# Kernel optimization log

Hardware: AMD Instinct MI355X
Metric: run time of the kernel (lower is better)

The kernel has to match this reference:

```python
import jax, jax.numpy as jnp
import numpy as np

N_HEADS = 4
DIM_HEAD = 32


def setup_inputs() -> dict:
    key = jax.random.key(0)
    k1, k2, k3, k4 = jax.random.split(key, 4)
    x = jax.random.normal(k1, (8, 64, 80, 1024), dtype=jnp.float32)
    # conv_qkv: 1x1 conv, no bias -> weight [3*heads*dim_head, dim_in_out]
    w_qkv = jax.random.normal(k2, (3 * N_HEADS * DIM_HEAD, 64), dtype=jnp.float32) * 0.05
    # conv_out: 1x1 conv with bias -> weight [dim_in_out, heads*dim_head], bias [dim_in_out]
    w_out = jax.random.normal(k3, (64, N_HEADS * DIM_HEAD), dtype=jnp.float32) * 0.05
    b_out = jax.random.normal(k4, (64,), dtype=jnp.float32) * 0.05
    return {"x": x, "w_qkv": w_qkv, "w_out": w_out, "b_out": b_out}


def reference(x, w_qkv, w_out, b_out):
    b, c, h, w = x.shape
    n = h * w
    # 1x1 conv == channel matmul
    qkv = jnp.einsum('bchw,oc->bohw', x, w_qkv)            # [b, 3*heads*dh, h, w]
    qkv = qkv.reshape(b, 3, N_HEADS, DIM_HEAD, n)          # qkv outermost, then heads, then c
    q, k, v = qkv[:, 0], qkv[:, 1], qkv[:, 2]              # each [b, heads, dh, n]
    k = jax.nn.softmax(k, axis=-1)                          # softmax over spatial positions
    context = jnp.einsum('bhdn,bhen->bhde', k, v)          # [b, heads, dh, dh]
    out = jnp.einsum('bhde,bhdn->bhen', context, q)        # [b, heads, dh, n]
    out = out.reshape(b, N_HEADS * DIM_HEAD, h, w)
    return jnp.einsum('bchw,oc->bohw', out, w_out) + b_out[None, :, None, None]
```

## Files before the change

kernel.cpp:

```cpp
#include <hip/hip_runtime.h>
#include <stdint.h>


#define N_POS 81920
#define NT    128
#define TILES 640

typedef short bf16x8 __attribute__((ext_vector_type(8)));
typedef float f32x4  __attribute__((ext_vector_type(4)));

__device__ __forceinline__ uint32_t packbf(float lo, float hi){
  uint32_t a = __float_as_uint(lo), b = __float_as_uint(hi);
  a = (a + 0x8000u) >> 16;
  b = (b + 0x8000u) & 0xffff0000u;
  return a | b;
}
__device__ __forceinline__ short bf16of(float v){
  return (short)((__float_as_uint(v) + 0x8000u) >> 16);
}

__global__ __launch_bounds__(512, 4) void kernA(
    const float* __restrict__ x, const float* __restrict__ w,
    float* __restrict__ pA, float* __restrict__ pZ, int nch, int tpc)
{
  __shared__ __align__(16) uint16_t xs_cp[64 * 136];
  __shared__ __align__(16) uint16_t xs_pc[128 * 72];
  __shared__ __align__(16) uint16_t es[128 * 136];

  const int t  = threadIdx.x;
  const int w8 = t >> 6;
  const int l  = t & 63;
  const int lm = l & 15;
  const int lg = l >> 4;

  const int b  = blockIdx.x / nch;
  const int ch = blockIdx.x % nch;
  const float* xb = x + (size_t)b * 64 * N_POS;

  const int rr  = t >> 3;
  const int pg  = t & 7;
  const int spp = t & 127;
  const int scg = t >> 7;

  const int pth = w8 & 3;
  const int ht0 = (w8 >> 2) * 4;

  bf16x8 wkf[4][2];
  #pragma unroll
  for (int i = 0; i < 4; ++i)
    #pragma unroll
    for (int kk = 0; kk < 2; ++kk){
      const float* wp = w + (size_t)(128 + 16*(ht0+i) + lm) * 64 + 32*kk + 8*lg;
      float4 w0 = *(const float4*)wp;
      float4 w1 = *(const float4*)(wp + 4);
      bf16x8 f;
      f[0]=bf16of(w0.x); f[1]=bf16of(w0.y); f[2]=bf16of(w0.z); f[3]=bf16of(w0.w);
      f[4]=bf16of(w1.x); f[5]=bf16of(w1.y); f[6]=bf16of(w1.z); f[7]=bf16of(w1.w);
      wkf[i][kk] = f;
    }

  bf16x8 ones;
  #pragma unroll
  for (int j = 0; j < 8; ++j) ones[j] = (short)0x3F80;

  f32x4 acc[4], zac;
  zac = (f32x4){0.f,0.f,0.f,0.f};
  #pragma unroll
  for (int n = 0; n < 4; ++n) acc[n] = (f32x4){0.f,0.f,0.f,0.f};

  float4 fa0, fa1, fa2, fa3;
  float v[16];
  {
    const int n0 = (ch * tpc) * NT;
    const float* ga = xb + (size_t)rr * N_POS + n0 + 16*pg;
    fa0 = *(const float4*)ga;       fa1 = *(const float4*)(ga + 4);
    fa2 = *(const float4*)(ga + 8); fa3 = *(const float4*)(ga + 12);
    const float* gb = xb + (size_t)(16*scg) * N_POS + n0 + spp;
    #pragma unroll
    for (int i = 0; i < 16; ++i) v[i] = gb[(size_t)i * N_POS];
  }

  for (int tile = 0; tile < tpc; ++tile){
    __syncthreads();
    {
      uint4 u0, u1;
      u0.x = packbf(fa0.x,fa0.y); u0.y = packbf(fa0.z,fa0.w);
      u0.z = packbf(fa1.x,fa1.y); u0.w = packbf(fa1.z,fa1.w);
      u1.x = packbf(fa2.x,fa2.y); u1.y = packbf(fa2.z,fa2.w);
      u1.z = packbf(fa3.x,fa3.y); u1.w = packbf(fa3.z,fa3.w);
      *(uint4*)&xs_cp[rr*136 + 16*pg]     = u0;
      *(uint4*)&xs_cp[rr*136 + 16*pg + 8] = u1;
      uint4 p0, p1;
      p0.x = packbf(v[0],v[1]);   p0.y = packbf(v[2],v[3]);
      p0.z = packbf(v[4],v[5]);   p0.w = packbf(v[6],v[7]);
      p1.x = packbf(v[8],v[9]);   p1.y = packbf(v[10],v[11]);
      p1.z = packbf(v[12],v[13]); p1.w = packbf(v[14],v[15]);
      *(uint4*)&xs_pc[spp*72 + 16*scg]     = p0;
      *(uint4*)&xs_pc[spp*72 + 16*scg + 8] = p1;
    }
    __syncthreads();
    if (tile + 1 < tpc){
      const int n1 = (ch * tpc + tile + 1) * NT;
      const float* ga = xb + (size_t)rr * N_POS + n1 + 16*pg;
      fa0 = *(const float4*)ga;       fa1 = *(const float4*)(ga + 4);
      fa2 = *(const float4*)(ga + 8); fa3 = *(const float4*)(ga + 12);
      const float* gb = xb + (size_t)(16*scg) * N_POS + n1 + spp;
      #pragma unroll
      for (int i = 0; i < 16; ++i) v[i] = gb[(size_t)i * N_POS];
    }
    #pragma unroll
    for (int ip = 0; ip < 2; ++ip){
      const int pt = pth + 4*ip;
      bf16x8 af0 = *(const bf16x8*)&xs_pc[(16*pt + lm)*72 + 8*lg];
      bf16x8 af1 = *(const bf16x8*)&xs_pc[(16*pt + lm)*72 + 32 + 8*lg];
      #pragma unroll
      for (int i = 0; i < 4; ++i){
        f32x4 s = (f32x4){0.f,0.f,0.f,0.f};
        s = __builtin_amdgcn_mfma_f32_16x16x32_bf16(af0, wkf[i][0], s, 0,0,0);
        s = __builtin_amdgcn_mfma_f32_16x16x32_bf16(af1, wkf[i][1], s, 0,0,0);
        float e0 = __expf(s[0]), e1 = __expf(s[1]);
        float e2 = __expf(s[2]), e3 = __expf(s[3]);
        uint2 pk; pk.x = packbf(e0,e1); pk.y = packbf(e2,e3);
        *(uint2*)&es[(16*(ht0+i) + lm)*136 + 16*pt + 4*lg] = pk;
      }
    }
    __syncthreads();
    __builtin_amdgcn_s_setprio(1);
    #pragma unroll
    for (int kk = 0; kk < 4; ++kk){
      bf16x8 ea = *(const bf16x8*)&es[(16*w8 + lm)*136 + 32*kk + 8*lg];
      bf16x8 xbf[4];
      #pragma unroll
      for (int n = 0; n < 4; ++n)
        xbf[n] = *(const bf16x8*)&xs_cp[(16*n + lm)*136 + 32*kk + 8*lg];
      #pragma unroll
      for (int n = 0; n < 4; ++n)
        acc[n] = __builtin_amdgcn_mfma_f32_16x16x32_bf16(ea, xbf[n], acc[n], 0,0,0);
      zac = __builtin_amdgcn_mfma_f32_16x16x32_bf16(ea, ones, zac, 0,0,0);
    }
    __builtin_amdgcn_s_setprio(0);
  }

  float* pa = pA + (size_t)blockIdx.x * 8192;
  const int hd0 = 16*w8 + 4*lg;
  #pragma unroll
  for (int n = 0; n < 4; ++n)
    #pragma unroll
    for (int r = 0; r < 4; ++r)
      pa[(size_t)(hd0 + r)*64 + 16*n + lm] = acc[n][r];
  if (lm == 0){
    #pragma unroll
    for (int r = 0; r < 4; ++r)
      pZ[(size_t)blockIdx.x * 128 + hd0 + r] = zac[r];
  }
}

__global__ __launch_bounds__(256) void kernR1(
    const float* __restrict__ pA, const float* __restrict__ pZ,
    float* __restrict__ Ar, float* __restrict__ Zr, int nch)
{
  const int b = blockIdx.x >> 3, s = blockIdx.x & 7;
  const int off = s * 1024 + threadIdx.x * 4;
  float4 a = make_float4(0.f, 0.f, 0.f, 0.f);
  for (int ch = 0; ch < nch; ++ch){
    float4 v = *(const float4*)&pA[(size_t)(b * nch + ch) * 8192 + off];
    a.x += v.x; a.y += v.y; a.z += v.z; a.w += v.w;
  }
  *(float4*)&Ar[(size_t)b * 8192 + off] = a;
  if (s == 0 && threadIdx.x < 128){
    float z = 0.f;
    for (int ch = 0; ch < nch; ++ch) z += pZ[(size_t)(b * nch + ch) * 128 + threadIdx.x];
    Zr[b * 128 + threadIdx.x] = z;
  }
}

__global__ __launch_bounds__(256) void kernCM(
    const float* __restrict__ Ar, const float* __restrict__ Zr,
    const float* __restrict__ w_qkv, const float* __restrict__ w_out,
    float* __restrict__ M)
{
  __shared__ float A[128 * 65];
  __shared__ float Z[128];
  __shared__ float cs[128 * 33];
  __shared__ float T[64 * 129];
  const int b = blockIdx.x, t = threadIdx.x;

  #pragma unroll
  for (int k = 0; k < 32; ++k){
    int i = t + 256 * k;
    A[(i >> 6) * 65 + (i & 63)] = Ar[(size_t)b * 8192 + i];
  }
  if (t < 128) Z[t] = Zr[b * 128 + t];
  __syncthreads();

  {
    const int hd = t & 127, h = hd >> 5, e0 = (t >> 7) * 16;
    const float rz = 1.0f / Z[hd];
    for (int je = 0; je < 16; ++je){
      int e = e0 + je;
      const float* wv = w_qkv + (size_t)(256 + 32 * h + e) * 64;
      float a = 0.f;
      #pragma unroll
      for (int c = 0; c < 64; ++c) a = fmaf(A[hd * 65 + c], wv[c], a);
      cs[hd * 33 + e] = a * rz;
    }
  }
  __syncthreads();

  const int o = t & 63, g = t >> 6;
  for (int jh = 0; jh < 32; ++jh){
    int hd = 32 * g + jh;
    const float* wo = w_out + (size_t)o * 128 + 32 * g;
    float a = 0.f;
    #pragma unroll
    for (int e = 0; e < 32; ++e) a = fmaf(wo[e], cs[hd * 33 + e], a);
    T[o * 129 + hd] = a;
  }
  __syncthreads();

  const int c0 = 16 * g;
  float m[16];
  #pragma unroll
  for (int j = 0; j < 16; ++j) m[j] = 0.f;
  for (int hd = 0; hd < 128; ++hd){
    float tv = T[o * 129 + hd];
    const float* wq = w_qkv + (size_t)hd * 64 + c0;
    #pragma unroll
    for (int j = 0; j < 16; ++j) m[j] = fmaf(tv, wq[j], m[j]);
  }
  #pragma unroll
  for (int j = 0; j < 16; ++j) M[(size_t)b * 4096 + o * 64 + c0 + j] = m[j];
}

__global__ __launch_bounds__(256, 4) void kernO(
    const float* __restrict__ x, const float* __restrict__ M,
    const float* __restrict__ b_out, float* __restrict__ out)
{
  const int t  = threadIdx.x;
  const int wv = t >> 6;
  const int l  = t & 63;
  const int lm = l & 15;
  const int lg = l >> 4;

  const int b  = blockIdx.x / 320;
  const int p0 = (blockIdx.x % 320) * 256;
  const float* xb = x + (size_t)b * 64 * N_POS + p0;

  const float* Mb = M + (size_t)b * 4096;
  bf16x8 mb[4][2];
  float bias[4];
  #pragma unroll
  for (int ot = 0; ot < 4; ++ot){
    bias[ot] = b_out[16*ot + lm];
    #pragma unroll
    for (int kk = 0; kk < 2; ++kk){
      const float* mp = Mb + (size_t)(16*ot + lm)*64 + 32*kk + 8*lg;
      float4 m0 = *(const float4*)mp;
      float4 m1 = *(const float4*)(mp + 4);
      bf16x8 f;
      f[0]=bf16of(m0.x); f[1]=bf16of(m0.y); f[2]=bf16of(m0.z); f[3]=bf16of(m0.w);
      f[4]=bf16of(m1.x); f[5]=bf16of(m1.y); f[6]=bf16of(m1.z); f[7]=bf16of(m1.w);
      mb[ot][kk] = f;
    }
  }

  float* ob = out + (size_t)b * 64 * N_POS + p0;

  #pragma unroll
  for (int ip = 0; ip < 4; ++ip){
    const int pt = 4*wv + ip;
    const float* gx = xb + 16*pt + lm;
    float a0[8], a1[8];
    #pragma unroll
    for (int j = 0; j < 8; ++j){
      a0[j] = gx[(size_t)(8*lg + j) * N_POS];
      a1[j] = gx[(size_t)(32 + 8*lg + j) * N_POS];
    }
    bf16x8 af0, af1;
    #pragma unroll
    for (int j = 0; j < 8; ++j){
      af0[j] = bf16of(a0[j]);
      af1[j] = bf16of(a1[j]);
    }
    #pragma unroll
    for (int ot = 0; ot < 4; ++ot){
      f32x4 d = (f32x4){0.f,0.f,0.f,0.f};
      d = __builtin_amdgcn_mfma_f32_16x16x32_bf16(af0, mb[ot][0], d, 0,0,0);
      d = __builtin_amdgcn_mfma_f32_16x16x32_bf16(af1, mb[ot][1], d, 0,0,0);
      float4 st = make_float4(d[0]+bias[ot], d[1]+bias[ot],
                              d[2]+bias[ot], d[3]+bias[ot]);
      *(float4*)&ob[(size_t)(16*ot + lm) * N_POS + 16*pt + 4*lg] = st;
    }
  }
}

extern "C" void kernel_launch(void* const* d_in, const int* in_sizes, int n_in,
                              void* d_out, int out_size, void* d_ws, size_t ws_size,
                              hipStream_t stream)
{
  const float* x     = (const float*)d_in[0];
  const float* w_qkv = (const float*)d_in[1];
  const float* w_out = (const float*)d_in[2];
  const float* b_out = (const float*)d_in[3];
  float* out = (float*)d_out;
  float* ws  = (float*)d_ws;

  static const int cand[] = {64, 40, 32, 20, 16, 10, 8, 5, 4, 2, 1};
  int nch = 1;
  for (int i = 0; i < 11; ++i){
    size_t need = ((size_t)8 * cand[i] * (8192 + 128)
                   + 8 * 8192 + 8 * 128 + (size_t)8 * 4096) * 4;
    if (need <= ws_size){ nch = cand[i]; break; }
  }
  const int tpc = TILES / nch;

  float* pA  = ws;
  float* pZ  = pA + (size_t)8 * nch * 8192;
  float* Ar  = pZ + (size_t)8 * nch * 128;
  float* Zr  = Ar + (size_t)8 * 8192;
  float* M   = Zr + (size_t)8 * 128;

  kernA<<<8 * nch, 512, 0, stream>>>(x, w_qkv, pA, pZ, nch, tpc);
  kernR1<<<64,     256, 0, stream>>>(pA, pZ, Ar, Zr, nch);
  kernCM<<<8,      256, 0, stream>>>(Ar, Zr, w_qkv, w_out, M);
  kernO<<<2560,    256, 0, stream>>>(x, M, b_out, out);
}
```

Before: 231.1 us.

## Stage bf16 position-major copy of x in kernA and reuse it in kernO

kernA now writes its already-converted bf16 tile of x, laid out position-major, to a workspace buffer. kernO reads that compact copy with vectorised contiguous loads instead of re-reading fp32 x with strided per-channel loads and converting it. This halves the bytes kernO reads. In exchange kernA takes on an extra global write, and the workspace requirement grows, which could force a smaller chunk count.

```diff
diff --git a/kernel.cpp b/kernel.cpp
--- a/kernel.cpp
+++ b/kernel.cpp
@@ -21,7 +21,8 @@
 
 __global__ __launch_bounds__(512, 4) void kernA(
     const float* __restrict__ x, const float* __restrict__ w,
-    float* __restrict__ pA, float* __restrict__ pZ, int nch, int tpc)
+    float* __restrict__ pA, float* __restrict__ pZ,
+    uint16_t* __restrict__ x16, int nch, int tpc)
 {
   __shared__ __align__(16) uint16_t xs_cp[64 * 136];
   __shared__ __align__(16) uint16_t xs_pc[128 * 72];
@@ -81,6 +82,7 @@
   }
 
   for (int tile = 0; tile < tpc; ++tile){
+    const int n0 = (ch * tpc + tile) * NT;
     __syncthreads();
     {
       uint4 u0, u1;
@@ -100,13 +102,21 @@
     }
     __syncthreads();
     if (tile + 1 < tpc){
-      const int n1 = (ch * tpc + tile + 1) * NT;
+      const int n1 = n0 + NT;
       const float* ga = xb + (size_t)rr * N_POS + n1 + 16*pg;
       fa0 = *(const float4*)ga;       fa1 = *(const float4*)(ga + 4);
       fa2 = *(const float4*)(ga + 8); fa3 = *(const float4*)(ga + 12);
       const float* gb = xb + (size_t)(16*scg) * N_POS + n1 + spp;
       #pragma unroll
       for (int i = 0; i < 16; ++i) v[i] = gb[(size_t)i * N_POS];
+    }
+    {
+      const int pos = t >> 2, q = t & 3;
+      uint4 q0 = *(const uint4*)&xs_pc[pos*72 + 16*q];
+      uint4 q1 = *(const uint4*)&xs_pc[pos*72 + 16*q + 8];
+      uint16_t* dst = x16 + ((size_t)b * N_POS + n0 + pos) * 64 + 16*q;
+      *(uint4*)&dst[0] = q0;
+      *(uint4*)&dst[8] = q1;
     }
     #pragma unroll
     for (int ip = 0; ip < 2; ++ip){
@@ -233,7 +243,7 @@
 }
 
 __global__ __launch_bounds__(256, 4) void kernO(
-    const float* __restrict__ x, const float* __restrict__ M,
+    const uint16_t* __restrict__ x16, const float* __restrict__ M,
     const float* __restrict__ b_out, float* __restrict__ out)
 {
   const int t  = threadIdx.x;
@@ -244,7 +254,7 @@
 
   const int b  = blockIdx.x / 320;
   const int p0 = (blockIdx.x % 320) * 256;
-  const float* xb = x + (size_t)b * 64 * N_POS + p0;
+  const uint16_t* xb = x16 + ((size_t)b * N_POS + p0) * 64;
 
   const float* Mb = M + (size_t)b * 4096;
   bf16x8 mb[4][2];
@@ -264,29 +274,24 @@
     }
   }
 
+  bf16x8 af0[4], af1[4];
+  #pragma unroll
+  for (int ip = 0; ip < 4; ++ip){
+    const int row = 16*(4*wv + ip) + lm;
+    af0[ip] = *(const bf16x8*)&xb[row*64 + 8*lg];
+    af1[ip] = *(const bf16x8*)&xb[row*64 + 32 + 8*lg];
+  }
+
   float* ob = out + (size_t)b * 64 * N_POS + p0;
 
   #pragma unroll
   for (int ip = 0; ip < 4; ++ip){
     const int pt = 4*wv + ip;
-    const float* gx = xb + 16*pt + lm;
-    float a0[8], a1[8];
-    #pragma unroll
-    for (int j = 0; j < 8; ++j){
-      a0[j] = gx[(size_t)(8*lg + j) * N_POS];
-      a1[j] = gx[(size_t)(32 + 8*lg + j) * N_POS];
-    }
-    bf16x8 af0, af1;
-    #pragma unroll
-    for (int j = 0; j < 8; ++j){
-      af0[j] = bf16of(a0[j]);
-      af1[j] = bf16of(a1[j]);
-    }
     #pragma unroll
     for (int ot = 0; ot < 4; ++ot){
       f32x4 d = (f32x4){0.f,0.f,0.f,0.f};
-      d = __builtin_amdgcn_mfma_f32_16x16x32_bf16(af0, mb[ot][0], d, 0,0,0);
-      d = __builtin_amdgcn_mfma_f32_16x16x32_bf16(af1, mb[ot][1], d, 0,0,0);
+      d = __builtin_amdgcn_mfma_f32_16x16x32_bf16(af0[ip], mb[ot][0], d, 0,0,0);
+      d = __builtin_amdgcn_mfma_f32_16x16x32_bf16(af1[ip], mb[ot][1], d, 0,0,0);
       float4 st = make_float4(d[0]+bias[ot], d[1]+bias[ot],
                               d[2]+bias[ot], d[3]+bias[ot]);
       *(float4*)&ob[(size_t)(16*ot + lm) * N_POS + 16*pt + 4*lg] = st;
@@ -305,11 +310,12 @@
   float* out = (float*)d_out;
   float* ws  = (float*)d_ws;
 
+  const size_t x16_bytes = (size_t)8 * N_POS * 64 * 2;
   static const int cand[] = {64, 40, 32, 20, 16, 10, 8, 5, 4, 2, 1};
   int nch = 1;
   for (int i = 0; i < 11; ++i){
     size_t need = ((size_t)8 * cand[i] * (8192 + 128)
-                   + 8 * 8192 + 8 * 128 + (size_t)8 * 4096) * 4;
+                   + 8 * 8192 + 8 * 128 + (size_t)8 * 4096) * 4 + x16_bytes;
     if (need <= ws_size){ nch = cand[i]; break; }
   }
   const int tpc = TILES / nch;
@@ -319,9 +325,10 @@
   float* Ar  = pZ + (size_t)8 * nch * 128;
   float* Zr  = Ar + (size_t)8 * 8192;
   float* M   = Zr + (size_t)8 * 128;
-
-  kernA<<<8 * nch, 512, 0, stream>>>(x, w_qkv, pA, pZ, nch, tpc);
+  uint16_t* x16 = (uint16_t*)(M + (size_t)8 * 4096);
+
+  kernA<<<8 * nch, 512, 0, stream>>>(x, w_qkv, pA, pZ, x16, nch, tpc);
   kernR1<<<64,     256, 0, stream>>>(pA, pZ, Ar, Zr, nch);
   kernCM<<<8,      256, 0, stream>>>(Ar, Zr, w_qkv, w_out, M);
-  kernO<<<2560,    256, 0, stream>>>(x, M, b_out, out);
-}
+  kernO<<<2560,    256, 0, stream>>>(x16, M, b_out, out);
+}
```

After: 215.8 us. -6.6%, faster.
